# Kernel tuning notes

Hardware: AMD Instinct MI355X
Metric: run time of the kernel (lower is better)

## Reference

```python
import jax, jax.numpy as jnp
import numpy as np

VARIANCES = jnp.array([0.1, 0.1, 0.2, 0.2], jnp.float32)
TOTAL_LABELS = 81
MAX_TOTAL = 200        # max_total_size (also max_output_size_per_class)
SCORE_T = 0.5          # score_threshold
IOU_T = 0.5            # tf combined_non_max_suppression default iou_threshold


def setup_inputs() -> dict:
    key = jax.random.key(0)
    k1, k2, k3, k4 = jax.random.split(key, 4)
    B, N, C = 8, 1000, TOTAL_LABELS
    # valid normalized RoIs: y1,x1 in [0,0.7), h,w in [0.01,0.31)
    yx1 = jax.random.uniform(k1, (B, N, 2), jnp.float32) * 0.7
    hw = jax.random.uniform(k2, (B, N, 2), jnp.float32) * 0.3 + 0.01
    roi_bboxes = jnp.concatenate([yx1, yx1 + hw], axis=-1)  # [y1,x1,y2,x2]
    pred_deltas = jax.random.normal(k3, (B, N, C * 4), jnp.float32) * 0.5
    pred_label_probs = jax.random.uniform(k4, (B, N, C), jnp.float32)
    return {"roi_bboxes": roi_bboxes, "pred_deltas": pred_deltas,
            "pred_label_probs": pred_label_probs}


def _decode(rois, deltas):
    # rois: [..., 4] (y1,x1,y2,x2); deltas: [..., 4] (dy,dx,dh,dw)
    h = rois[..., 2] - rois[..., 0]
    w = rois[..., 3] - rois[..., 1]
    cy = rois[..., 0] + 0.5 * h
    cx = rois[..., 1] + 0.5 * w
    ncy = deltas[..., 0] * h + cy
    ncx = deltas[..., 1] * w + cx
    nh = jnp.exp(deltas[..., 2]) * h
    nw = jnp.exp(deltas[..., 3]) * w
    return jnp.stack([ncy - 0.5 * nh, ncx - 0.5 * nw,
                      ncy + 0.5 * nh, ncx + 0.5 * nw], axis=-1)


def _nms_lane(boxes, scores):
    # greedy per-class NMS over one (batch, class) lane. boxes [N,4], scores [N]
    N = boxes.shape[0]
    order = jnp.argsort(-scores)
    b = boxes[order]
    s = scores[order]
    area = (b[:, 2] - b[:, 0]) * (b[:, 3] - b[:, 1])
    idx = jnp.arange(N)

    def body(i, keep):
        bi = b[i]
        iy1 = jnp.maximum(bi[0], b[:, 0])
        ix1 = jnp.maximum(bi[1], b[:, 1])
        iy2 = jnp.minimum(bi[2], b[:, 2])
        ix2 = jnp.minimum(bi[3], b[:, 3])
        inter = jnp.maximum(iy2 - iy1, 0.0) * jnp.maximum(ix2 - ix1, 0.0)
        iou = inter / (area[i] + area - inter + 1e-8)
        suppress = keep[i] & (iou > IOU_T) & (idx > i)
        return keep & ~suppress

    keep0 = s > SCORE_T                       # score filtering before NMS
    keep = jax.lax.fori_loop(0, N, body, keep0)
    keep = keep & (jnp.cumsum(keep) <= MAX_TOTAL)  # max_output_size_per_class
    return b, jnp.where(keep, s, 0.0)          # boxes in score order, masked scores


def _forward(roi_bboxes, pred_deltas, pred_label_probs):
    B, N, _ = pred_deltas.shape
    C = TOTAL_LABELS
    deltas = pred_deltas.reshape(B, N, C, 4) * VARIANCES
    boxes = _decode(roi_bboxes[:, :, None, :], deltas)          # [B,N,C,4]
    bg = jnp.argmax(pred_label_probs, axis=-1)[..., None] == 0  # background rows
    scores = jnp.where(bg, 0.0, pred_label_probs)               # [B,N,C]

    boxes_t = boxes.transpose(0, 2, 1, 3)   # [B,C,N,4]
    scores_t = scores.transpose(0, 2, 1)    # [B,C,N]
    b_s, s_s = jax.vmap(jax.vmap(_nms_lane))(boxes_t, scores_t)

    flat_s = s_s.reshape(B, C * N)
    flat_b = b_s.reshape(B, C * N, 4)
    cls = jnp.broadcast_to(jnp.arange(C)[:, None], (C, N)).reshape(C * N)

    top_s, top_i = jax.lax.top_k(flat_s, MAX_TOTAL)             # combined top-k
    top_b = jnp.take_along_axis(flat_b, top_i[..., None], axis=1)
    top_c = cls[top_i]

    valid = top_s > 0.0
    final_b = jnp.clip(jnp.where(valid[..., None], top_b, 0.0), 0.0, 1.0)
    final_c = jnp.where(valid, top_c, 0).astype(jnp.float32)
    final_s = jnp.where(valid, top_s, 0.0)
    return final_b, final_c, final_s


def reference(roi_bboxes, pred_deltas, pred_label_probs):
    return _forward(roi_bboxes, pred_deltas, pred_label_probs)
```

## Files before the change

kernel.cpp:

```cpp
#include <hip/hip_runtime.h>

#define NROI 1000
#define NCLS 81
#define NB   8
#define NLANE (NB*NCLS)
#define MAXM 1024
#define MAXKEEP 200
#define SCORE_T 0.5f
#define NT 512
#define NW 8
#define SCAP 1024

typedef unsigned long long u64;
typedef unsigned int u32;


__device__ __forceinline__ void decode_box(const float* __restrict__ roi,
                                           const float* __restrict__ dl,
                                           float& oy1, float& ox1,
                                           float& oy2, float& ox2) {
#pragma clang fp contract(off)
  float y1 = roi[0], x1 = roi[1], y2 = roi[2], x2 = roi[3];
  float h = y2 - y1;
  float w = x2 - x1;
  float cy = y1 + 0.5f * h;
  float cx = x1 + 0.5f * w;
  float d0 = dl[0] * 0.1f;
  float d1 = dl[1] * 0.1f;
  float d2 = dl[2] * 0.2f;
  float d3 = dl[3] * 0.2f;
  float ncy = d0 * h + cy;
  float ncx = d1 * w + cx;
  float nh = expf(d2) * h;
  float nw = expf(d3) * w;
  oy1 = ncy - 0.5f * nh;
  ox1 = ncx - 0.5f * nw;
  oy2 = ncy + 0.5f * nh;
  ox2 = ncx + 0.5f * nw;
}

__device__ __forceinline__ float area_f(float4 bx) {
#pragma clang fp contract(off)
  return (bx.z - bx.x) * (bx.w - bx.y);
}

__device__ __forceinline__ bool hit_f(float4 bi, float ia, float4 bj, float ja) {
#pragma clang fp contract(off)
  float yy1 = fmaxf(bi.x, bj.x);
  float xx1 = fmaxf(bi.y, bj.y);
  float yy2 = fminf(bi.z, bj.z);
  float xx2 = fminf(bi.w, bj.w);
  float ih = fmaxf(yy2 - yy1, 0.0f);
  float iw = fmaxf(xx2 - xx1, 0.0f);
  float inter = ih * iw;
  float den = ia + ja;
  den = den - inter;
  den = den + 1e-8f;
  return (inter + inter) > den;
}

__device__ __forceinline__ u64 pack_key(u32 sbits, int flat, int n) {
  return ((u64)sbits << 32) | ((u64)(131071 - flat) << 15) | ((u64)n << 5);
}

__global__ __launch_bounds__(256) void bg_kernel(const float* __restrict__ probs,
                                                 int* __restrict__ bg,
                                                 int* __restrict__ bhist) {
  if (blockIdx.x < 8) {
    bhist[blockIdx.x * 256 + threadIdx.x] = 0;
  }
  int row = blockIdx.x * 4 + (threadIdx.x >> 6);
  int lane = threadIdx.x & 63;
  if (row >= NB * NROI) return;
  const float* p = probs + (size_t)row * NCLS;
  float m = -1e30f;
  for (int idx = 1 + lane; idx < NCLS; idx += 64) m = fmaxf(m, p[idx]);
  for (int off = 32; off; off >>= 1) m = fmaxf(m, __shfl_xor(m, off));
  if (lane == 0) bg[row] = (p[0] >= m) ? 1 : 0;
}

__global__ __launch_bounds__(NT) void gather_nms_kernel(
    const float* __restrict__ roi, const float* __restrict__ deltas,
    const float* __restrict__ probs, const int* __restrict__ bg,
    int* __restrict__ keep_count, u64* __restrict__ lane_key,
    int* __restrict__ bhist) {
  int lane = (blockIdx.x % 8) * NCLS + blockIdx.x / 8;
  int b = lane / NCLS, c = lane % NCLS;
  int tid = threadIdx.x;
  int w = tid >> 6, l = tid & 63;

  __shared__ alignas(16) char smem[26624];
  float4* sbox   = (float4*)smem;
  u64*    skeyU  = (u64*)smem;
  u64*    skeyB  = (u64*)(smem + 8192);
  u64*    skey   = (u64*)(smem + 16384);
  int*    bcnt   = (int*)(smem + 24576);
  int*    bstart = (int*)(smem + 25600);
  __shared__ float4 klist[320];
  __shared__ u64 hmask8[2][NW][64];
  __shared__ u64 suppm8[2][NW];
  __shared__ u64 keepmask[16];
  __shared__ int scount, segbase[16];

  if (tid == 0) scount = 0;
  if (tid < 256) bcnt[tid] = 0;
  __syncthreads();

  for (int base_n = 0; base_n < NROI; base_n += NT) {
    int n = base_n + tid;
    bool cand = false;
    float s = 0.0f;
    if (n < NROI) {
      int row = b * NROI + n;
      s = probs[(size_t)row * NCLS + c];
      cand = (s > SCORE_T) && (bg[row] == 0);
    }
    u64 bal = __ballot(cand);
    int wb = 0;
    if (l == 0) wb = atomicAdd(&scount, (int)__popcll(bal));
    wb = __shfl(wb, 0);
    if (cand) {
      int off = (int)__popcll(bal & ((1ull << l) - 1ull));
      u32 sb = __float_as_uint(s);
      skeyU[wb + off] = ((u64)sb << 32) | (u64)(0xFFFFFFFFu - (u32)n);
      atomicAdd(&bcnt[(sb >> 15) & 255], 1);
    }
  }
  __syncthreads();
  int M = scount;
  int nchunks = (M + 63) >> 6;

  if (w == 0) {
    int d0 = 4 * l, d1 = d0 + 1, d2 = d0 + 2, d3 = d0 + 3;
    int c0 = bcnt[255 - d0], c1 = bcnt[255 - d1];
    int c2 = bcnt[255 - d2], c3 = bcnt[255 - d3];
    int t = c0 + c1 + c2 + c3;
    int inc = t;
    for (int off = 1; off < 64; off <<= 1) {
      int v = __shfl_up(inc, off);
      if (l >= off) inc += v;
    }
    int excl = inc - t;
    int s0 = excl, s1 = excl + c0, s2 = excl + c0 + c1, s3 = excl + c0 + c1 + c2;
    bcnt[255 - d0] = s0; bstart[255 - d0] = s0;
    bcnt[255 - d1] = s1; bstart[255 - d1] = s1;
    bcnt[255 - d2] = s2; bstart[255 - d2] = s2;
    bcnt[255 - d3] = s3; bstart[255 - d3] = s3;
  }
  __syncthreads();

  for (int p = tid; p < M; p += NT) {
    u64 k = skeyU[p];
    int bkt = (int)((k >> 47) & 255);
    int pos = atomicAdd(&bcnt[bkt], 1);
    skeyB[pos] = k;
  }
  __syncthreads();

  for (int p = tid; p < M; p += NT) {
    u64 k = skeyB[p];
    int bkt = (int)((k >> 47) & 255);
    int st = bstart[bkt], en = bcnt[bkt];
    int r = st;
    for (int q = st; q < en; ++q) r += (skeyB[q] > k) ? 1 : 0;
    skey[r] = k;
  }
  if (tid < 16) {
    int rem = M - (tid << 6);
    keepmask[tid] = (rem >= 64) ? ~0ull : ((rem <= 0) ? 0ull : ((1ull << rem) - 1ull));
  }
  __syncthreads();

  if (w == 7 && nchunks > 0) {
    u64 k = skey[l];
    int nn = (int)(0xFFFFFFFFu - (u32)(k & 0xFFFFFFFFull));
    int row = b * NROI + ((l < M) ? nn : 0);
    float by1, bx1, by2, bx2;
    decode_box(roi + (size_t)row * 4, deltas + ((size_t)row * NCLS + c) * 4,
               by1, bx1, by2, bx2);
    sbox[l] = make_float4(by1, bx1, by2, bx2);
  }
  __syncthreads();

  int kc = 0;
  int par = 0;
  const u64 low = (1ull << l) - 1ull;
  for (int ck = 0; ck < nchunks; ++ck) {
    int start = ck << 6;
    float4 bj = sbox[start + l];
    float ja = area_f(bj);

    {
      u64 part = 0;
#pragma unroll
      for (int r = 0; r < 8; ++r) {
        int i = (w << 3) + r;
        float4 bi = sbox[start + i];
        float ia = area_f(bi);
        if (hit_f(bi, ia, bj, ja)) part |= (1ull << i);
      }
      hmask8[par][w][l] = part;
    }

    {
      bool supp = false;
      for (int i = w; i < kc; i += NW) {
        float4 bi = klist[i];
        float ia = area_f(bi);
        supp |= hit_f(bi, ia, bj, ja);
      }
      u64 sb = __ballot(supp);
      if (l == 0) suppm8[par][w] = sb;
    }

    if (w == 7 && ck + 1 < nchunks) {
      int p = ((ck + 1) << 6) + l;
      u64 k = skey[p];
      int nn = (int)(0xFFFFFFFFu - (u32)(k & 0xFFFFFFFFull));
      int row = b * NROI + ((p < M) ? nn : 0);
      float by1, bx1, by2, bx2;
      decode_box(roi + (size_t)row * 4, deltas + ((size_t)row * NCLS + c) * 4,
                 by1, bx1, by2, bx2);
      sbox[p] = make_float4(by1, bx1, by2, bx2);
    }
    __syncthreads();

    u64 rowm = hmask8[par][0][l] | hmask8[par][1][l] | hmask8[par][2][l]
             | hmask8[par][3][l] | hmask8[par][4][l] | hmask8[par][5][l]
             | hmask8[par][6][l] | hmask8[par][7][l];
    u64 sall = suppm8[par][0] | suppm8[par][1] | suppm8[par][2] | suppm8[par][3]
             | suppm8[par][4] | suppm8[par][5] | suppm8[par][6] | suppm8[par][7];
    int rem0 = M - start;
    u64 alive = (rem0 >= 64) ? ~0ull : ((rem0 <= 0) ? 0ull : ((1ull << rem0) - 1ull));
    u64 und = alive & ~sall;
    u64 kept = 0;
    while (und) {
      bool isu = (und >> l) & 1;
      bool su = isu && ((rowm & kept & low) != 0ull);
      bool ke = isu && ((rowm & (kept | und) & low) == 0ull);
      u64 sm = __ballot(su);
      u64 km2 = __ballot(ke);
      kept |= km2;
      und &= ~(sm | km2);
    }
    if ((kept >> l) & 1) {
      klist[kc + (int)__popcll(kept & low)] = bj;
    }
    if (tid == 0) keepmask[ck] = kept;
    kc += (int)__popcll(kept);
    if (kc >= MAXKEEP) break;
    par ^= 1;
  }
  __syncthreads();

  if (tid < 16) {
    int acc = 0;
    for (int i = 0; i < tid; ++i) acc += (int)__popcll(keepmask[i]);
    segbase[tid] = acc;
  }
  if (tid < 256) bcnt[tid] = 0;
  __syncthreads();
  int total = segbase[15] + (int)__popcll(keepmask[15]);
  for (int s = 0; s < 2; ++s) {
    int seg = (w << 1) + s;
    u64 word = keepmask[seg];
    int p = (seg << 6) + l;
    if ((word >> l) & 1) {
      int rank = segbase[seg] + (int)__popcll(word & ((1ull << l) - 1ull));
      if (rank < MAXKEEP) {
        u64 k = skey[p];
        u32 sbits = (u32)(k >> 32);
        int n = (int)(0xFFFFFFFFu - (u32)(k & 0xFFFFFFFFull));
        lane_key[(size_t)lane * MAXKEEP + rank] = pack_key(sbits, c * NROI + p, n);
        atomicAdd(&bcnt[(int)((sbits >> 15) & 255)], 1);
      }
    }
  }
  __syncthreads();
  if (tid < 256 && bcnt[tid] != 0)
    atomicAdd(&bhist[b * 256 + tid], bcnt[tid]);
  if (tid == 0) keep_count[lane] = min(total, MAXKEEP);
}

__global__ __launch_bounds__(512) void merge_kernel(
    const float* __restrict__ roi, const float* __restrict__ deltas,
    const int* __restrict__ keep_count, const u64* __restrict__ lane_key,
    const int* __restrict__ bhist,
    float* __restrict__ out_b, float* __restrict__ out_c, float* __restrict__ out_s) {
  int b = blockIdx.x;
  int tid = threadIdx.x;
  int w = tid >> 6, l = tid & 63;

  __shared__ int mhist[256];
  __shared__ int mhsuf[256];
  __shared__ int mhcur[256];
  __shared__ int mcnts[NCLS];
  __shared__ int mtot, mscnt;
  __shared__ u64 msurv[SCAP];

  if (tid < 256) mhist[tid] = bhist[b * 256 + tid];
  for (int i = tid; i < NCLS; i += 512) mcnts[i] = keep_count[b * NCLS + i];
  if (tid == 0) mscnt = 0;
  for (int t = tid; t < MAXKEEP; t += 512) {
    size_t ob = ((size_t)b * MAXKEEP + t) * 4;
    out_b[ob + 0] = 0.0f; out_b[ob + 1] = 0.0f;
    out_b[ob + 2] = 0.0f; out_b[ob + 3] = 0.0f;
    out_c[b * MAXKEEP + t] = 0.0f;
    out_s[b * MAXKEEP + t] = 0.0f;
  }
  __syncthreads();

  if (w == 0) {
    int g0 = 4 * l;
    int c0 = mhist[g0], c1 = mhist[g0 + 1], c2 = mhist[g0 + 2], c3 = mhist[g0 + 3];
    int t = c0 + c1 + c2 + c3;
    int acc = t;
    for (int off = 1; off < 64; off <<= 1) {
      int v = __shfl_down(acc, off);
      if (l + off < 64) acc += v;
    }
    if (l == 0) mtot = acc;
    int above = acc - t;
    int s3 = above, s2 = above + c3, s1 = above + c3 + c2, s0 = above + c3 + c2 + c1;
    mhsuf[g0 + 3] = s3; mhcur[g0 + 3] = s3;
    mhsuf[g0 + 2] = s2; mhcur[g0 + 2] = s2;
    mhsuf[g0 + 1] = s1; mhcur[g0 + 1] = s1;
    mhsuf[g0 + 0] = s0; mhcur[g0 + 0] = s0;
  }
  __syncthreads();
  int valid = (mtot < MAXKEEP) ? mtot : MAXKEEP;

  for (int s = tid; s < NCLS * MAXKEEP; s += 512) {
    int c2 = s / MAXKEEP, h = s % MAXKEEP;
    if (h < mcnts[c2]) {
      u64 k = lane_key[((size_t)(b * NCLS + c2)) * MAXKEEP + h];
      int bkt = (int)((k >> 47) & 255);
      if (mhsuf[bkt] < MAXKEEP) {
        int pos = atomicAdd(&mhcur[bkt], 1);
        if (pos < SCAP) { msurv[pos] = k; atomicAdd(&mscnt, 1); }
      }
    }
  }
  __syncthreads();
  int scnt = min(mscnt, SCAP);

  for (int p = tid; p < scnt; p += 512) {
    u64 k = msurv[p];
    int bkt = (int)((k >> 47) & 255);
    int st = mhsuf[bkt];
    int en = st + mhist[bkt];
    if (en > SCAP) en = SCAP;
    int r = st;
    for (int q = st; q < en; ++q) r += (msurv[q] > k) ? 1 : 0;
    if (r < valid) {
      int flat = 131071 - (int)((k >> 15) & 0x1FFFF);
      int c2 = flat / NROI;
      int n = (int)((k >> 5) & 0x3FF);
      int row = b * NROI + n;
      float by1, bx1, by2, bx2;
      decode_box(roi + (size_t)row * 4, deltas + ((size_t)row * NCLS + c2) * 4,
                 by1, bx1, by2, bx2);
      size_t ob = ((size_t)b * MAXKEEP + r) * 4;
      out_b[ob + 0] = fminf(fmaxf(by1, 0.0f), 1.0f);
      out_b[ob + 1] = fminf(fmaxf(bx1, 0.0f), 1.0f);
      out_b[ob + 2] = fminf(fmaxf(by2, 0.0f), 1.0f);
      out_b[ob + 3] = fminf(fmaxf(bx2, 0.0f), 1.0f);
      out_c[b * MAXKEEP + r] = (float)c2;
      out_s[b * MAXKEEP + r] = __uint_as_float((u32)(k >> 32));
    }
  }
}

extern "C" void kernel_launch(void* const* d_in, const int* in_sizes, int n_in,
                              void* d_out, int out_size, void* d_ws, size_t ws_size,
                              hipStream_t stream) {
  const float* roi    = (const float*)d_in[0];
  const float* deltas = (const float*)d_in[1];
  const float* probs  = (const float*)d_in[2];

  char* ws = (char*)d_ws;
  int* bg         = (int*)(ws);
  int* bhist      = (int*)(ws + 32768);
  int* keep_count = (int*)(ws + 40960);
  u64* lane_key   = (u64*)(ws + 45056);

  float* out_b = (float*)d_out;
  float* out_c = out_b + NB * MAXKEEP * 4;
  float* out_s = out_c + NB * MAXKEEP;

  bg_kernel<<<(NB * NROI + 3) / 4, 256, 0, stream>>>(probs, bg, bhist);
  gather_nms_kernel<<<NLANE, NT, 0, stream>>>(roi, deltas, probs, bg,
                                              keep_count, lane_key, bhist);
  merge_kernel<<<NB, 512, 0, stream>>>(roi, deltas, keep_count, lane_key, bhist,
                                       out_b, out_c, out_s);
}
```

Measured before the change: 61.37 us.

## Fuse background detection into NMS kernel and build score histogram in merge

Removes the separate background-argmax kernel. Each NMS block now recomputes the background mask for its batch's 1000 rows into a shared bitmask, so every one of 81 class blocks redundantly reads the whole batch's probability rows. The score histogram used for top-k selection is no longer accumulated with global atomics in the NMS kernel; the merge kernel builds it from the kept keys instead. The goal is to drop a kernel launch and the global atomic traffic, at the cost of redundant probability reads per block and extra serial work in the 8-block merge.

```diff
diff --git a/kernel.cpp b/kernel.cpp
--- a/kernel.cpp
+++ b/kernel.cpp
@@ -63,27 +63,10 @@
   return ((u64)sbits << 32) | ((u64)(131071 - flat) << 15) | ((u64)n << 5);
 }
 
-__global__ __launch_bounds__(256) void bg_kernel(const float* __restrict__ probs,
-                                                 int* __restrict__ bg,
-                                                 int* __restrict__ bhist) {
-  if (blockIdx.x < 8) {
-    bhist[blockIdx.x * 256 + threadIdx.x] = 0;
-  }
-  int row = blockIdx.x * 4 + (threadIdx.x >> 6);
-  int lane = threadIdx.x & 63;
-  if (row >= NB * NROI) return;
-  const float* p = probs + (size_t)row * NCLS;
-  float m = -1e30f;
-  for (int idx = 1 + lane; idx < NCLS; idx += 64) m = fmaxf(m, p[idx]);
-  for (int off = 32; off; off >>= 1) m = fmaxf(m, __shfl_xor(m, off));
-  if (lane == 0) bg[row] = (p[0] >= m) ? 1 : 0;
-}
-
 __global__ __launch_bounds__(NT) void gather_nms_kernel(
     const float* __restrict__ roi, const float* __restrict__ deltas,
-    const float* __restrict__ probs, const int* __restrict__ bg,
-    int* __restrict__ keep_count, u64* __restrict__ lane_key,
-    int* __restrict__ bhist) {
+    const float* __restrict__ probs,
+    int* __restrict__ keep_count, u64* __restrict__ lane_key) {
   int lane = (blockIdx.x % 8) * NCLS + blockIdx.x / 8;
   int b = lane / NCLS, c = lane % NCLS;
   int tid = threadIdx.x;
@@ -100,10 +83,39 @@
   __shared__ u64 hmask8[2][NW][64];
   __shared__ u64 suppm8[2][NW];
   __shared__ u64 keepmask[16];
+  __shared__ u64 bgmask[16];
   __shared__ int scount, segbase[16];
 
   if (tid == 0) scount = 0;
   if (tid < 256) bcnt[tid] = 0;
+
+  {
+    int g0 = w << 1, g1 = g0 | 1;
+    u64 m0 = 0, m1 = 0;
+    const size_t bb0 = (size_t)(b * NROI);
+    for (int j = 0; j < 64; ++j) {
+      int r0 = (g0 << 6) + j;
+      int r1 = (g1 << 6) + j;
+      int r1c = (r1 < NROI) ? r1 : (NROI - 1);
+      const float* p0r = probs + (bb0 + r0) * NCLS;
+      const float* p1r = probs + (bb0 + r1c) * NCLS;
+      float a0 = p0r[l];
+      float a1 = p1r[l];
+      float e0 = (l < 17) ? p0r[64 + l] : -1e30f;
+      float e1 = (l < 17) ? p1r[64 + l] : -1e30f;
+      float c0 = fmaxf((l == 0) ? -1e30f : a0, e0);
+      float c1 = fmaxf((l == 0) ? -1e30f : a1, e1);
+      for (int off = 32; off; off >>= 1) {
+        c0 = fmaxf(c0, __shfl_xor(c0, off));
+        c1 = fmaxf(c1, __shfl_xor(c1, off));
+      }
+      float z0 = __shfl(a0, 0);
+      float z1 = __shfl(a1, 0);
+      if (z0 >= c0) m0 |= (1ull << j);
+      if (z1 >= c1) m1 |= (1ull << j);
+    }
+    if (l == 0) { bgmask[g0] = m0; bgmask[g1] = m1; }
+  }
   __syncthreads();
 
   for (int base_n = 0; base_n < NROI; base_n += NT) {
@@ -111,9 +123,8 @@
     bool cand = false;
     float s = 0.0f;
     if (n < NROI) {
-      int row = b * NROI + n;
-      s = probs[(size_t)row * NCLS + c];
-      cand = (s > SCORE_T) && (bg[row] == 0);
+      s = probs[((size_t)(b * NROI + n)) * NCLS + c];
+      cand = (s > SCORE_T) && !((bgmask[n >> 6] >> (n & 63)) & 1);
     }
     u64 bal = __ballot(cand);
     int wb = 0;
@@ -258,7 +269,6 @@
     for (int i = 0; i < tid; ++i) acc += (int)__popcll(keepmask[i]);
     segbase[tid] = acc;
   }
-  if (tid < 256) bcnt[tid] = 0;
   __syncthreads();
   int total = segbase[15] + (int)__popcll(keepmask[15]);
   for (int s = 0; s < 2; ++s) {
@@ -272,20 +282,15 @@
         u32 sbits = (u32)(k >> 32);
         int n = (int)(0xFFFFFFFFu - (u32)(k & 0xFFFFFFFFull));
         lane_key[(size_t)lane * MAXKEEP + rank] = pack_key(sbits, c * NROI + p, n);
-        atomicAdd(&bcnt[(int)((sbits >> 15) & 255)], 1);
       }
     }
   }
-  __syncthreads();
-  if (tid < 256 && bcnt[tid] != 0)
-    atomicAdd(&bhist[b * 256 + tid], bcnt[tid]);
   if (tid == 0) keep_count[lane] = min(total, MAXKEEP);
 }
 
 __global__ __launch_bounds__(512) void merge_kernel(
     const float* __restrict__ roi, const float* __restrict__ deltas,
     const int* __restrict__ keep_count, const u64* __restrict__ lane_key,
-    const int* __restrict__ bhist,
     float* __restrict__ out_b, float* __restrict__ out_c, float* __restrict__ out_s) {
   int b = blockIdx.x;
   int tid = threadIdx.x;
@@ -298,7 +303,7 @@
   __shared__ int mtot, mscnt;
   __shared__ u64 msurv[SCAP];
 
-  if (tid < 256) mhist[tid] = bhist[b * 256 + tid];
+  if (tid < 256) mhist[tid] = 0;
   for (int i = tid; i < NCLS; i += 512) mcnts[i] = keep_count[b * NCLS + i];
   if (tid == 0) mscnt = 0;
   for (int t = tid; t < MAXKEEP; t += 512) {
@@ -307,6 +312,15 @@
     out_b[ob + 2] = 0.0f; out_b[ob + 3] = 0.0f;
     out_c[b * MAXKEEP + t] = 0.0f;
     out_s[b * MAXKEEP + t] = 0.0f;
+  }
+  __syncthreads();
+
+  for (int s = tid; s < NCLS * MAXKEEP; s += 512) {
+    int c2 = s / MAXKEEP, h = s % MAXKEEP;
+    if (h < mcnts[c2]) {
+      u64 k = lane_key[((size_t)(b * NCLS + c2)) * MAXKEEP + h];
+      atomicAdd(&mhist[(int)((k >> 47) & 255)], 1);
+    }
   }
   __syncthreads();
 
@@ -379,18 +393,15 @@
   const float* probs  = (const float*)d_in[2];
 
   char* ws = (char*)d_ws;
-  int* bg         = (int*)(ws);
-  int* bhist      = (int*)(ws + 32768);
-  int* keep_count = (int*)(ws + 40960);
-  u64* lane_key   = (u64*)(ws + 45056);
+  int* keep_count = (int*)(ws);
+  u64* lane_key   = (u64*)(ws + 4096);
 
   float* out_b = (float*)d_out;
   float* out_c = out_b + NB * MAXKEEP * 4;
   float* out_s = out_c + NB * MAXKEEP;
 
-  bg_kernel<<<(NB * NROI + 3) / 4, 256, 0, stream>>>(probs, bg, bhist);
-  gather_nms_kernel<<<NLANE, NT, 0, stream>>>(roi, deltas, probs, bg,
-                                              keep_count, lane_key, bhist);
-  merge_kernel<<<NB, 512, 0, stream>>>(roi, deltas, keep_count, lane_key, bhist,
+  gather_nms_kernel<<<NLANE, NT, 0, stream>>>(roi, deltas, probs,
+                                              keep_count, lane_key);
+  merge_kernel<<<NB, 512, 0, stream>>>(roi, deltas, keep_count, lane_key,
                                        out_b, out_c, out_s);
 }
```

New measurement: 122.1 us. 1.99x slower.
